# Performance work log

Measured on AMD Instinct MI355X. Metric: run time of the kernel, lower is better.

The kernel has to match this reference:

```python
import jax, jax.numpy as jnp
import numpy as np

B, S, H, K, L, NH, FF = 4, 2048, 2048, 1024, 2, 16, 4096
EPS = 1e-5

def _alibi_slopes(n):
    # standard power-of-two ALiBi slopes
    start = 2.0 ** (-8.0 / n)
    return start ** jnp.arange(1, n + 1, dtype=jnp.float32)

def _layernorm(h, g, b):
    mu = jnp.mean(h, axis=-1, keepdims=True)
    var = jnp.mean(jnp.square(h - mu), axis=-1, keepdims=True)
    return (h - mu) * jax.lax.rsqrt(var + EPS) * g + b

def setup_inputs() -> dict:
    key = jax.random.key(0)
    ks = jax.random.split(key, 16)
    x = jax.random.normal(ks[0], (B, S, H), jnp.float32)
    prev = jax.random.normal(ks[1], (B, S, H), jnp.float32)
    # unique sorted token indices per batch row (jit-friendly boolean mask)
    idx = jnp.stack([jnp.sort(jax.random.permutation(jax.random.fold_in(ks[2], b), S)[:K])
                     for b in range(B)]).astype(jnp.int32)
    w = 0.02
    Wq = jax.random.normal(ks[3], (L, H, H), jnp.float32) * w
    Wk = jax.random.normal(ks[4], (L, H, H), jnp.float32) * w
    Wv = jax.random.normal(ks[5], (L, H, H), jnp.float32) * w
    Wo = jax.random.normal(ks[6], (L, H, H), jnp.float32) * w
    attn_gamma = jnp.ones((L, H), jnp.float32)
    attn_beta = jnp.zeros((L, H), jnp.float32)
    mlp_gamma = jnp.ones((L, H), jnp.float32)
    mlp_beta = jnp.zeros((L, H), jnp.float32)
    Wgate = jax.random.normal(ks[7], (L, H, FF), jnp.float32) * w
    Wup = jax.random.normal(ks[8], (L, H, FF), jnp.float32) * w
    Wdown = jax.random.normal(ks[9], (L, FF, H), jnp.float32) * w
    return {"x": x, "prev": prev, "idx": idx, "Wq": Wq, "Wk": Wk, "Wv": Wv,
            "Wo": Wo, "attn_gamma": attn_gamma, "attn_beta": attn_beta,
            "mlp_gamma": mlp_gamma, "mlp_beta": mlp_beta,
            "Wgate": Wgate, "Wup": Wup, "Wdown": Wdown}

def _forward(x, prev, idx, Wq, Wk, Wv, Wo, attn_gamma, attn_beta,
             mlp_gamma, mlp_beta, Wgate, Wup, Wdown):
    d = H // NH
    scale = 1.0 / jnp.sqrt(jnp.asarray(d, jnp.float32))
    # gather selected tokens: [B, K, H]
    cur = jnp.take_along_axis(x, idx[:, :, None], axis=1)
    mem = jnp.take_along_axis(prev, idx[:, :, None], axis=1)
    # non-causal ALiBi bias over selected-sequence positions: [NH, K, K]
    pos = jnp.arange(K)
    dist = jnp.abs(pos[:, None] - pos[None, :]).astype(jnp.float32)
    bias = -_alibi_slopes(NH)[:, None, None] * dist
    for l in range(L):
        q = (cur @ Wq[l]).reshape(B, K, NH, d)
        k = (mem @ Wk[l]).reshape(B, K, NH, d)
        v = (mem @ Wv[l]).reshape(B, K, NH, d)
        scores = jnp.einsum('bqhd,bkhd->bhqk', q, k) * scale + bias
        attn = jax.nn.softmax(scores, axis=-1)
        o = jnp.einsum('bhqk,bkhd->bqhd', attn, v).reshape(B, K, H) @ Wo[l]
        cur = cur + o
        normed = _layernorm(cur, attn_gamma[l], attn_beta[l])
        mlp = (jax.nn.silu(normed @ Wgate[l]) * (normed @ Wup[l])) @ Wdown[l]
        cur = cur + mlp
        cur = _layernorm(cur, mlp_gamma[l], mlp_beta[l])
    # scatter-add back: out[mask] += update_val
    out = x.at[jnp.arange(B)[:, None], idx].add(cur)
    return out

def reference(x, prev, idx, Wq, Wk, Wv, Wo, attn_gamma, attn_beta,
              mlp_gamma, mlp_beta, Wgate, Wup, Wdown):
    return _forward(x, prev, idx, Wq, Wk, Wv, Wo, attn_gamma, attn_beta,
                    mlp_gamma, mlp_beta, Wgate, Wup, Wdown)
```

## Files before the change

kernel.cpp:

```cpp
#include <hip/hip_runtime.h>
#include <hip/hip_bf16.h>

#define BB 4
#define SS 2048
#define HH 2048
#define KK 1024
#define LL 2
#define NHH 16
#define FFF 4096
#define DD 128

typedef __attribute__((ext_vector_type(8))) short s8v;
typedef __attribute__((ext_vector_type(4))) short s4v;
typedef __attribute__((ext_vector_type(4))) float f4v;

__device__ __forceinline__ short f2bf(float f) {
  unsigned u = __builtin_bit_cast(unsigned, f);
  u += 0x7fffu + ((u >> 16) & 1u);
  return (short)(u >> 16);
}
__device__ __forceinline__ float bf2f(short s) {
  unsigned u = ((unsigned)(unsigned short)s) << 16;
  return __builtin_bit_cast(float, u);
}
__device__ __forceinline__ f4v mfma16(s8v a, s8v b, f4v c) {
  asm("v_mfma_f32_16x16x32_bf16 %0, %1, %2, %0" : "+v"(c) : "v"(a), "v"(b));
  return c;
}
__device__ __forceinline__ void gload_lds16(const void* g, void* l) {
  __builtin_amdgcn_global_load_lds(
      (__attribute__((address_space(1))) void*)g,
      (__attribute__((address_space(3))) void*)l, 16, 0, 0);
}
template <int N>
__device__ __forceinline__ void barrier_cnt() {
  if constexpr (N == 3)
    asm volatile("s_waitcnt vmcnt(3) expcnt(0) lgkmcnt(0)" ::: "memory");
  else if constexpr (N == 4)
    asm volatile("s_waitcnt vmcnt(4) expcnt(0) lgkmcnt(0)" ::: "memory");
  else
    asm volatile("s_waitcnt vmcnt(0) expcnt(0) lgkmcnt(0)" ::: "memory");
  __builtin_amdgcn_s_barrier();
  asm volatile("" ::: "memory");
}

__global__ __launch_bounds__(256) void wconv(const float* __restrict__ W,
                                             short* __restrict__ Wt,
                                             int Kd, int N) {
  __shared__ short tile[64][65];
  int n0 = blockIdx.x * 64, k0 = blockIdx.y * 64;
  int t = threadIdx.x;
#pragma unroll
  for (int i = 0; i < 16; ++i) {
    int lin = i * 256 + t;
    int r = lin >> 6, c = lin & 63;
    tile[c][r] = f2bf(W[(size_t)(k0 + r) * N + n0 + c]);
  }
  __syncthreads();
#pragma unroll
  for (int i = 0; i < 16; ++i) {
    int lin = i * 256 + t;
    int r = lin >> 6, c = lin & 63;
    Wt[(size_t)(n0 + r) * Kd + k0 + c] = tile[r][c];
  }
}

__global__ __launch_bounds__(256) void gather_rows(
    const float* __restrict__ x, const float* __restrict__ prev,
    const int* __restrict__ idx, float* __restrict__ cur_f,
    short* __restrict__ cur_b, short* __restrict__ mem_b) {
  int r = blockIdx.x;
  int b = r >> 10, kk = r & (KK - 1);
  int src = idx[b * KK + kk];
  const float4* xs = (const float4*)(x + ((size_t)b * SS + src) * HH);
  const float4* ps = (const float4*)(prev + ((size_t)b * SS + src) * HH);
  float4* cf = (float4*)(cur_f + (size_t)r * HH);
  s4v* cb = (s4v*)(cur_b + (size_t)r * HH);
  s4v* mb = (s4v*)(mem_b + (size_t)r * HH);
  int t = threadIdx.x;
#pragma unroll
  for (int i = 0; i < 2; ++i) {
    int c = t + i * 256;
    float4 xv = xs[c], pv = ps[c];
    cf[c] = xv;
    s4v cv, mv;
    cv[0] = f2bf(xv.x); cv[1] = f2bf(xv.y); cv[2] = f2bf(xv.z); cv[3] = f2bf(xv.w);
    mv[0] = f2bf(pv.x); mv[1] = f2bf(pv.y); mv[2] = f2bf(pv.z); mv[3] = f2bf(pv.w);
    cb[c] = cv; mb[c] = mv;
  }
}

template <int EPI>
__global__ __launch_bounds__(512, 2) void g8p(
    const short* __restrict__ A, const short* __restrict__ Bt,
    float* __restrict__ Cf, short* __restrict__ Cb,
    const short* __restrict__ Other, int M, int N, int Kd) {
  __shared__ __align__(16) short smem[3 * 12288];
  const int t = threadIdx.x;
  const int w = t >> 6, l = t & 63;
  const int wr = w >> 2, wc = w & 3;
  const int l15 = l & 15, lh = l >> 4;
  const int koffs = (lh ^ ((l15 >> 1) & 3)) * 8;

  const int gx = gridDim.x, gy = gridDim.y;
  const int nwg = gx * gy;
  const int bid = blockIdx.y * gx + blockIdx.x;
  const int wg = (bid & 7) * (nwg >> 3) + (bid >> 3);
  const int by = wg & (gy - 1);
  const int bx = wg / gy;
  const int rowBase = by * 128, colBase = bx * 256;

  const int ar = t >> 2;
  const int ac = ((t & 3) ^ ((t >> 3) & 3)) * 8;
  const short* gA = A + (size_t)(rowBase + ar) * Kd + ac;
  const short* gB0 = Bt + (size_t)(colBase + ar) * Kd + ac;
  const short* gB1 = gB0 + (size_t)128 * Kd;
  const int lA = t * 8;
  const int lB = 4096 + t * 8;

  auto stage = [&](int bi, int kt) {
    const int k0 = kt * 32;
    short* base = smem + bi * 12288;
    gload_lds16(gA + k0, base + lA);
    gload_lds16(gB0 + k0, base + lB);
    gload_lds16(gB1 + k0, base + lB + 4096);
  };

  f4v acc[4][4];
#pragma unroll
  for (int i = 0; i < 4; ++i)
#pragma unroll
    for (int j = 0; j < 4; ++j) acc[i][j] = (f4v){0.f, 0.f, 0.f, 0.f};

  const int NT = Kd >> 5;
  stage(0, 0);
  stage(1, 1);
  barrier_cnt<3>();

  int cur = 0;
  for (int kt = 0; kt < NT; ++kt) {
    const short* sb = smem + cur * 12288;
    const bool more = (kt + 2 < NT);
    if (more) {
      int nb = cur + 2; if (nb >= 3) nb -= 3;
      stage(nb, kt + 2);
    }
    s8v af[4], bf[4];
#pragma unroll
    for (int mt = 0; mt < 4; ++mt)
      af[mt] = *(const s8v*)(sb + (wr * 64 + mt * 16 + l15) * 32 + koffs);
#pragma unroll
    for (int nt = 0; nt < 4; ++nt)
      bf[nt] = *(const s8v*)(sb + 4096 + (wc * 64 + nt * 16 + l15) * 32 + koffs);
#pragma unroll
    for (int mt = 0; mt < 4; ++mt)
#pragma unroll
      for (int nt = 0; nt < 4; ++nt)
        acc[mt][nt] = mfma16(af[mt], bf[nt], acc[mt][nt]);
    if (more) barrier_cnt<3>(); else barrier_cnt<0>();
    cur = (cur + 1 == 3) ? 0 : cur + 1;
  }

#pragma unroll
  for (int mt = 0; mt < 4; ++mt) {
#pragma unroll
    for (int nt = 0; nt < 4; ++nt) {
#pragma unroll
      for (int rr = 0; rr < 4; ++rr) {
        int row = rowBase + wr * 64 + mt * 16 + lh * 4 + rr;
        int col = colBase + wc * 64 + nt * 16 + l15;
        float v = acc[mt][nt][rr];
        if constexpr (EPI == 0) {
          Cb[(size_t)row * N + col] = f2bf(v);
        } else if constexpr (EPI == 1) {
          Cf[(size_t)row * N + col] += v;
        } else if constexpr (EPI == 2) {
          int b = row >> 10, ktok = row & (KK - 1);
          int h = col >> 7, dd = col & (DD - 1);
          Cb[(((size_t)(b * NHH + h)) * DD + dd) * KK + ktok] = f2bf(v);
        } else if constexpr (EPI == 3) {
          float sv = v / (1.f + __expf(-v));
          Cb[(size_t)row * N + col] = f2bf(sv);
        } else {
          float o = bf2f(Other[(size_t)row * N + col]);
          Cb[(size_t)row * N + col] = f2bf(v * o);
        }
      }
    }
  }
}

template <int EPI>
__global__ __launch_bounds__(512, 2) void g256(
    const short* __restrict__ A, const short* __restrict__ Bt,
    float* __restrict__ Cf, short* __restrict__ Cb,
    const short* __restrict__ Other, int M, int N, int Kd) {
  __shared__ __align__(16) short smem[3 * 16384];
  const int t = threadIdx.x;
  const int w = t >> 6, l = t & 63;
  const int wr = w >> 1, wc = w & 1;
  const int l15 = l & 15, lh = l >> 4;
  const int koffs = (lh ^ ((l15 >> 1) & 3)) * 8;

  const int gx = gridDim.x, gy = gridDim.y;
  const int nwg = gx * gy;
  const int bid = blockIdx.y * gx + blockIdx.x;
  const int wg = (bid & 7) * (nwg >> 3) + (bid >> 3);
  const int by = wg & (gy - 1);
  const int bx = wg / gy;
  const int rowBase = by * 256, colBase = bx * 256;

  const int ar = t >> 2;
  const int ac = ((t & 3) ^ ((t >> 3) & 3)) * 8;
  const short* gA = A + (size_t)(rowBase + ar) * Kd + ac;
  const short* gB = Bt + (size_t)(colBase + ar) * Kd + ac;
  const int lA = t * 8;
  const int lB = 8192 + t * 8;

  auto stage = [&](int bi, int kt) {
    const int k0 = kt * 32;
    short* base = smem + bi * 16384;
    gload_lds16(gA + k0, base + lA);
    gload_lds16(gA + k0 + (size_t)128 * Kd, base + lA + 4096);
    gload_lds16(gB + k0, base + lB);
    gload_lds16(gB + k0 + (size_t)128 * Kd, base + lB + 4096);
  };

  f4v acc[4][8];
#pragma unroll
  for (int i = 0; i < 4; ++i)
#pragma unroll
    for (int j = 0; j < 8; ++j) acc[i][j] = (f4v){0.f, 0.f, 0.f, 0.f};

  const int NT = Kd >> 5;
  stage(0, 0);
  stage(1, 1);
  barrier_cnt<4>();

  int cur = 0;
  for (int kt = 0; kt < NT; ++kt) {
    const short* sb = smem + cur * 16384;
    const bool more = (kt + 2 < NT);
    if (more) {
      int nb = cur + 2; if (nb >= 3) nb -= 3;
      stage(nb, kt + 2);
    }
    s8v af[4], bf[8];
#pragma unroll
    for (int mt = 0; mt < 4; ++mt)
      af[mt] = *(const s8v*)(sb + (wr * 64 + mt * 16 + l15) * 32 + koffs);
#pragma unroll
    for (int nt = 0; nt < 8; ++nt)
      bf[nt] = *(const s8v*)(sb + 8192 + (wc * 128 + nt * 16 + l15) * 32 + koffs);
#pragma unroll
    for (int mt = 0; mt < 4; ++mt)
#pragma unroll
      for (int nt = 0; nt < 8; ++nt)
        acc[mt][nt] = mfma16(af[mt], bf[nt], acc[mt][nt]);
    if (more) barrier_cnt<4>(); else barrier_cnt<0>();
    cur = (cur + 1 == 3) ? 0 : cur + 1;
  }

#pragma unroll
  for (int mt = 0; mt < 4; ++mt) {
#pragma unroll
    for (int nt = 0; nt < 8; ++nt) {
#pragma unroll
      for (int rr = 0; rr < 4; ++rr) {
        int row = rowBase + wr * 64 + mt * 16 + lh * 4 + rr;
        int col = colBase + wc * 128 + nt * 16 + l15;
        float v = acc[mt][nt][rr];
        if constexpr (EPI == 0) {
          Cb[(size_t)row * N + col] = f2bf(v);
        } else if constexpr (EPI == 1) {
          Cf[(size_t)row * N + col] += v;
        } else if constexpr (EPI == 3) {
          float sv = v / (1.f + __expf(-v));
          Cb[(size_t)row * N + col] = f2bf(sv);
        } else if constexpr (EPI == 4) {
          float o = bf2f(Other[(size_t)row * N + col]);
          Cb[(size_t)row * N + col] = f2bf(v * o);
        }
      }
    }
  }
}

__global__ __launch_bounds__(256, 2) void attn_fwd(
    const short* __restrict__ qb, const short* __restrict__ kb,
    const short* __restrict__ vT, short* __restrict__ ob) {
  __shared__ __align__(16) short Kl[64 * 136];
  __shared__ __align__(16) short Vl[128 * 72];
  __shared__ __align__(16) short Pl[64 * 72];
  int b = blockIdx.z, h = blockIdx.y, qt = blockIdx.x;
  int t = threadIdx.x, w = t >> 6, l = t & 63, l15 = l & 15, lh = l >> 4;
  const float LOG2E = 1.4426950408889634f;
  float slope2 = exp2f(-0.5f * (float)(h + 1)) * LOG2E;
  const float c1 = 0.08838834764831845f * LOG2E;

  s8v qf[4];
  int qrowA = qt * 64 + w * 16 + l15;
  const short* qptr = qb + ((size_t)(b * KK + qrowA)) * HH + h * DD + lh * 8;
#pragma unroll
  for (int ks = 0; ks < 4; ++ks) qf[ks] = *(const s8v*)(qptr + ks * 32);

  f4v oacc[8];
#pragma unroll
  for (int i = 0; i < 8; ++i) oacc[i] = (f4v){0.f, 0.f, 0.f, 0.f};
  float m[4], sden[4];
#pragma unroll
  for (int r = 0; r < 4; ++r) { m[r] = -1e30f; sden[r] = 0.f; }
  int qpos_base = qt * 64 + w * 16 + lh * 4;

  for (int kt = 0; kt < KK / 64; ++kt) {
    {
      int rr = t >> 4, cc = (t & 15) * 8;
#pragma unroll
      for (int it = 0; it < 4; ++it) {
        int krow = it * 16 + rr;
        s8v g = *(const s8v*)(kb + ((size_t)(b * KK + kt * 64 + krow)) * HH + h * DD + cc);
        *(s8v*)&Kl[krow * 136 + cc] = g;
      }
      int dr = t >> 3, c2 = (t & 7) * 8;
#pragma unroll
      for (int it = 0; it < 4; ++it) {
        int drow = it * 32 + dr;
        s8v g = *(const s8v*)(vT + (((size_t)(b * NHH + h)) * DD + drow) * KK + kt * 64 + c2);
        *(s8v*)&Vl[drow * 72 + c2] = g;
      }
    }
    __syncthreads();

    f4v sacc[4];
#pragma unroll
    for (int ct = 0; ct < 4; ++ct) sacc[ct] = (f4v){0.f, 0.f, 0.f, 0.f};
#pragma unroll
    for (int ct = 0; ct < 4; ++ct)
#pragma unroll
      for (int ks = 0; ks < 4; ++ks) {
        s8v kf = *(const s8v*)&Kl[(ct * 16 + l15) * 136 + ks * 32 + lh * 8];
        sacc[ct] = mfma16(qf[ks], kf, sacc[ct]);
      }

#pragma unroll
    for (int r = 0; r < 4; ++r) {
      int qpos = qpos_base + r;
      float mx = -1e30f;
#pragma unroll
      for (int ct = 0; ct < 4; ++ct) {
        int kpos = kt * 64 + ct * 16 + l15;
        float sv = sacc[ct][r] * c1 - slope2 * fabsf((float)(qpos - kpos));
        sacc[ct][r] = sv;
        mx = fmaxf(mx, sv);
      }
      mx = fmaxf(mx, __shfl_xor(mx, 1));
      mx = fmaxf(mx, __shfl_xor(mx, 2));
      mx = fmaxf(mx, __shfl_xor(mx, 4));
      mx = fmaxf(mx, __shfl_xor(mx, 8));
      float mn = fmaxf(m[r], mx);
      float corr = exp2f(m[r] - mn);
      m[r] = mn;
      float ps = 0.f;
#pragma unroll
      for (int ct = 0; ct < 4; ++ct) {
        float p = exp2f(sacc[ct][r] - mn);
        sacc[ct][r] = p;
        ps += p;
      }
      ps += __shfl_xor(ps, 1); ps += __shfl_xor(ps, 2);
      ps += __shfl_xor(ps, 4); ps += __shfl_xor(ps, 8);
      sden[r] = sden[r] * corr + ps;
#pragma unroll
      for (int dt = 0; dt < 8; ++dt) oacc[dt][r] *= corr;
#pragma unroll
      for (int ct = 0; ct < 4; ++ct)
        Pl[(w * 16 + lh * 4 + r) * 72 + ct * 16 + l15] = f2bf(sacc[ct][r]);
    }

#pragma unroll
    for (int ks2 = 0; ks2 < 2; ++ks2) {
      s8v pa = *(const s8v*)&Pl[(w * 16 + l15) * 72 + ks2 * 32 + lh * 8];
#pragma unroll
      for (int dt = 0; dt < 8; ++dt) {
        s8v vf = *(const s8v*)&Vl[(dt * 16 + l15) * 72 + ks2 * 32 + lh * 8];
        oacc[dt] = mfma16(pa, vf, oacc[dt]);
      }
    }
    __syncthreads();
  }

#pragma unroll
  for (int dt = 0; dt < 8; ++dt)
#pragma unroll
    for (int r = 0; r < 4; ++r) {
      int qpos = qpos_base + r;
      int dd = dt * 16 + l15;
      ob[((size_t)(b * KK + qpos)) * HH + h * DD + dd] = f2bf(oacc[dt][r] / sden[r]);
    }
}

__global__ __launch_bounds__(256) void ln_rows(const float* in,
    const float* __restrict__ gma, const float* __restrict__ bta,
    short* __restrict__ outb, float* outf) {
  __shared__ float red[2][4];
  int r = blockIdx.x, t = threadIdx.x;
  const float4* x4 = (const float4*)(in + (size_t)r * HH);
  float4 va = x4[t], vb = x4[t + 256];
  float sum = va.x + va.y + va.z + va.w + vb.x + vb.y + vb.z + vb.w;
  float sq = va.x * va.x + va.y * va.y + va.z * va.z + va.w * va.w +
             vb.x * vb.x + vb.y * vb.y + vb.z * vb.z + vb.w * vb.w;
#pragma unroll
  for (int off = 32; off; off >>= 1) {
    sum += __shfl_down(sum, off);
    sq += __shfl_down(sq, off);
  }
  int w = t >> 6;
  if ((t & 63) == 0) { red[0][w] = sum; red[1][w] = sq; }
  __syncthreads();
  sum = red[0][0] + red[0][1] + red[0][2] + red[0][3];
  sq = red[1][0] + red[1][1] + red[1][2] + red[1][3];
  float mu = sum * (1.f / HH);
  float rs = rsqrtf(sq * (1.f / HH) - mu * mu + 1e-5f);
  const float4* g4 = (const float4*)gma;
  const float4* b4 = (const float4*)bta;
  s4v* ob = (s4v*)(outb + (size_t)r * HH);
  float4* of = (float4*)(outf ? outf + (size_t)r * HH : nullptr);
#pragma unroll
  for (int i = 0; i < 2; ++i) {
    int c = t + i * 256;
    float4 v = (i == 0) ? va : vb;
    float4 g = g4[c], bb = b4[c];
    float4 nv;
    nv.x = (v.x - mu) * rs * g.x + bb.x;
    nv.y = (v.y - mu) * rs * g.y + bb.y;
    nv.z = (v.z - mu) * rs * g.z + bb.z;
    nv.w = (v.w - mu) * rs * g.w + bb.w;
    s4v o;
    o[0] = f2bf(nv.x); o[1] = f2bf(nv.y); o[2] = f2bf(nv.z); o[3] = f2bf(nv.w);
    ob[c] = o;
    if (outf) of[c] = nv;
  }
}

__global__ __launch_bounds__(256) void copy_out(const float* __restrict__ x,
                                                float* __restrict__ out, size_t n4) {
  size_t i = (size_t)blockIdx.x * 256 + threadIdx.x;
  size_t stride = (size_t)gridDim.x * 256;
  const float4* xi = (const float4*)x;
  float4* oi = (float4*)out;
  for (; i < n4; i += stride) oi[i] = xi[i];
}

__global__ __launch_bounds__(256) void scatter_add(const int* __restrict__ idx,
                                                   const float* __restrict__ cur,
                                                   float* out) {
  int r = blockIdx.x;
  int b = r >> 10, kk = r & (KK - 1);
  int dst = idx[b * KK + kk];
  float4* o = (float4*)(out + ((size_t)b * SS + dst) * HH);
  const float4* c = (const float4*)(cur + (size_t)r * HH);
  int t = threadIdx.x;
#pragma unroll
  for (int i = 0; i < 2; ++i) {
    int j = t + i * 256;
    float4 ov = o[j], cv = c[j];
    ov.x += cv.x; ov.y += cv.y; ov.z += cv.z; ov.w += cv.w;
    o[j] = ov;
  }
}

extern "C" void kernel_launch(void* const* d_in, const int* in_sizes, int n_in,
                              void* d_out, int out_size, void* d_ws, size_t ws_size,
                              hipStream_t stream) {
  (void)in_sizes; (void)n_in; (void)out_size; (void)ws_size;
  const float* x = (const float*)d_in[0];
  const float* prv = (const float*)d_in[1];
  const int* idx = (const int*)d_in[2];
  const float* Wq = (const float*)d_in[3];
  const float* Wk = (const float*)d_in[4];
  const float* Wv = (const float*)d_in[5];
  const float* Wo = (const float*)d_in[6];
  const float* ag = (const float*)d_in[7];
  const float* ab = (const float*)d_in[8];
  const float* mg = (const float*)d_in[9];
  const float* mbt = (const float*)d_in[10];
  const float* Wg = (const float*)d_in[11];
  const float* Wu = (const float*)d_in[12];
  const float* Wd = (const float*)d_in[13];
  float* out = (float*)d_out;

  char* ws = (char*)d_ws;
  size_t off = 0;
  auto alloc = [&](size_t bytes) -> void* {
    void* p = ws + off;
    off += (bytes + 255) & ~(size_t)255;
    return p;
  };
  const size_t WHH = (size_t)HH * HH, WHF = (size_t)HH * FFF;
  short* WqT = (short*)alloc(LL * WHH * 2);
  short* WkT = (short*)alloc(LL * WHH * 2);
  short* WvT = (short*)alloc(LL * WHH * 2);
  short* WoT = (short*)alloc(LL * WHH * 2);
  short* WgT = (short*)alloc(LL * WHF * 2);
  short* WuT = (short*)alloc(LL * WHF * 2);
  short* WdT = (short*)alloc(LL * WHF * 2);
  const size_t RH = (size_t)BB * KK * HH;
  float* cur_f = (float*)alloc(RH * 4);
  short* q_b = (short*)alloc(RH * 2);
  short* k_b = (short*)alloc(RH * 2);
  short* vT_b = (short*)alloc(RH * 2);
  short* o_b = (short*)alloc(RH * 2);
  short* cur_b = (short*)alloc(RH * 2);
  short* mem_b = (short*)alloc(RH * 2);
  short* nrm_b = (short*)alloc(RH * 2);
  short* sg_b = q_b;
  short* hid_b = vT_b;

  dim3 blk(256), blk512(512);
  for (int l = 0; l < LL; ++l) {
    wconv<<<dim3(HH / 64, HH / 64), blk, 0, stream>>>(Wq + l * WHH, WqT + l * WHH, HH, HH);
    wconv<<<dim3(HH / 64, HH / 64), blk, 0, stream>>>(Wk + l * WHH, WkT + l * WHH, HH, HH);
    wconv<<<dim3(HH / 64, HH / 64), blk, 0, stream>>>(Wv + l * WHH, WvT + l * WHH, HH, HH);
    wconv<<<dim3(HH / 64, HH / 64), blk, 0, stream>>>(Wo + l * WHH, WoT + l * WHH, HH, HH);
    wconv<<<dim3(FFF / 64, HH / 64), blk, 0, stream>>>(Wg + l * WHF, WgT + l * WHF, HH, FFF);
    wconv<<<dim3(FFF / 64, HH / 64), blk, 0, stream>>>(Wu + l * WHF, WuT + l * WHF, HH, FFF);
    wconv<<<dim3(HH / 64, FFF / 64), blk, 0, stream>>>(Wd + l * WHF, WdT + l * WHF, FFF, HH);
  }
  gather_rows<<<dim3(BB * KK), blk, 0, stream>>>(x, prv, idx, cur_f, cur_b, mem_b);

  const int M = BB * KK;
  for (int l = 0; l < LL; ++l) {
    const short* wq = WqT + l * WHH;
    const short* wk = WkT + l * WHH;
    const short* wv = WvT + l * WHH;
    const short* wo = WoT + l * WHH;
    const short* wg_ = WgT + l * WHF;
    const short* wu = WuT + l * WHF;
    const short* wd = WdT + l * WHF;
    g8p<0><<<dim3(HH / 256, M / 128), blk512, 0, stream>>>(cur_b, wq, nullptr, q_b, nullptr, M, HH, HH);
    g8p<0><<<dim3(HH / 256, M / 128), blk512, 0, stream>>>(mem_b, wk, nullptr, k_b, nullptr, M, HH, HH);
    g8p<2><<<dim3(HH / 256, M / 128), blk512, 0, stream>>>(mem_b, wv, nullptr, vT_b, nullptr, M, HH, HH);
    attn_fwd<<<dim3(KK / 64, NHH, BB), blk, 0, stream>>>(q_b, k_b, vT_b, o_b);
    g8p<1><<<dim3(HH / 256, M / 128), blk512, 0, stream>>>(o_b, wo, cur_f, nullptr, nullptr, M, HH, HH);
    ln_rows<<<dim3(M), blk, 0, stream>>>(cur_f, ag + l * HH, ab + l * HH, nrm_b, nullptr);
    g256<3><<<dim3(FFF / 256, M / 256), blk512, 0, stream>>>(nrm_b, wg_, nullptr, sg_b, nullptr, M, FFF, HH);
    g256<4><<<dim3(FFF / 256, M / 256), blk512, 0, stream>>>(nrm_b, wu, nullptr, hid_b, sg_b, M, FFF, HH);
    g8p<1><<<dim3(HH / 256, M / 128), blk512, 0, stream>>>(hid_b, wd, cur_f, nullptr, nullptr, M, HH, FFF);
    ln_rows<<<dim3(M), blk, 0, stream>>>(cur_f, mg + l * HH, mbt + l * HH, cur_b, cur_f);
  }
  copy_out<<<dim3(2048), blk, 0, stream>>>(x, out, (size_t)BB * SS * HH / 4);
  scatter_add<<<dim3(M), blk, 0, stream>>>(idx, cur_f, out);
}
```

Measured before the change: 1.309 ms.

## Fuse K/V and gate/up projections into single wide GEMMs, use fast exp2

Result: no change. 1.319 ms (+0.8%).

```diff
diff --git a/kernel.cpp b/kernel.cpp
--- a/kernel.cpp
+++ b/kernel.cpp
@@ -94,7 +94,7 @@
 __global__ __launch_bounds__(512, 2) void g8p(
     const short* __restrict__ A, const short* __restrict__ Bt,
     float* __restrict__ Cf, short* __restrict__ Cb,
-    const short* __restrict__ Other, int M, int N, int Kd) {
+    int M, int N, int Kd) {
   __shared__ __align__(16) short smem[3 * 12288];
   const int t = threadIdx.x;
   const int w = t >> 6, l = t & 63;
@@ -178,12 +178,6 @@
           int b = row >> 10, ktok = row & (KK - 1);
           int h = col >> 7, dd = col & (DD - 1);
           Cb[(((size_t)(b * NHH + h)) * DD + dd) * KK + ktok] = f2bf(v);
-        } else if constexpr (EPI == 3) {
-          float sv = v / (1.f + __expf(-v));
-          Cb[(size_t)row * N + col] = f2bf(sv);
-        } else {
-          float o = bf2f(Other[(size_t)row * N + col]);
-          Cb[(size_t)row * N + col] = f2bf(v * o);
         }
       }
     }
@@ -193,8 +187,7 @@
 template <int EPI>
 __global__ __launch_bounds__(512, 2) void g256(
     const short* __restrict__ A, const short* __restrict__ Bt,
-    float* __restrict__ Cf, short* __restrict__ Cb,
-    const short* __restrict__ Other, int M, int N, int Kd) {
+    short* __restrict__ Cb, short* __restrict__ Cb2, int M, int N, int Kd) {
   __shared__ __align__(16) short smem[3 * 16384];
   const int t = threadIdx.x;
   const int w = t >> 6, l = t & 63;
@@ -270,22 +263,48 @@
         int row = rowBase + wr * 64 + mt * 16 + lh * 4 + rr;
         int col = colBase + wc * 128 + nt * 16 + l15;
         float v = acc[mt][nt][rr];
-        if constexpr (EPI == 0) {
-          Cb[(size_t)row * N + col] = f2bf(v);
-        } else if constexpr (EPI == 1) {
-          Cf[(size_t)row * N + col] += v;
-        } else if constexpr (EPI == 3) {
-          float sv = v / (1.f + __expf(-v));
-          Cb[(size_t)row * N + col] = f2bf(sv);
-        } else if constexpr (EPI == 4) {
-          float o = bf2f(Other[(size_t)row * N + col]);
-          Cb[(size_t)row * N + col] = f2bf(v * o);
+        if constexpr (EPI == 5) {
+          if (col < HH) {
+            Cb[(size_t)row * HH + col] = f2bf(v);
+          } else {
+            int vcol = col - HH;
+            int b = row >> 10, ktok = row & (KK - 1);
+            int h = vcol >> 7, dd = vcol & (DD - 1);
+            Cb2[(((size_t)(b * NHH + h)) * DD + dd) * KK + ktok] = f2bf(v);
+          }
+        } else if constexpr (EPI == 6) {
+          if (col < FFF) {
+            float sv = v / (1.f + __expf(-v));
+            Cb[(size_t)row * FFF + col] = f2bf(sv);
+          } else {
+            Cb2[(size_t)row * FFF + (col - FFF)] = f2bf(v);
+          }
         }
       }
     }
   }
 }
 
+__global__ __launch_bounds__(256) void mul_bf16(short* __restrict__ hid,
+                                                const short* __restrict__ sg,
+                                                size_t n8) {
+  size_t i = (size_t)blockIdx.x * 256 + threadIdx.x;
+  size_t stride = (size_t)gridDim.x * 256;
+  for (; i < n8; i += stride) {
+    s8v a = ((const s8v*)hid)[i];
+    s8v b = ((const s8v*)sg)[i];
+    s8v o;
+#pragma unroll
+    for (int j = 0; j < 8; ++j) o[j] = f2bf(bf2f(a[j]) * bf2f(b[j]));
+    ((s8v*)hid)[i] = o;
+  }
+}
+
+__device__ __forceinline__ float exp2fast(float x) {
+  float r;
+  asm("v_exp_f32 %0, %1\n\ts_nop 0" : "=v"(r) : "v"(x));
+  return r;
+}
 __global__ __launch_bounds__(256, 2) void attn_fwd(
     const short* __restrict__ qb, const short* __restrict__ kb,
     const short* __restrict__ vT, short* __restrict__ ob) {
@@ -358,12 +377,12 @@
       mx = fmaxf(mx, __shfl_xor(mx, 4));
       mx = fmaxf(mx, __shfl_xor(mx, 8));
       float mn = fmaxf(m[r], mx);
-      float corr = exp2f(m[r] - mn);
+      float corr = exp2fast(m[r] - mn);
       m[r] = mn;
       float ps = 0.f;
 #pragma unroll
       for (int ct = 0; ct < 4; ++ct) {
-        float p = exp2f(sacc[ct][r] - mn);
+        float p = exp2fast(sacc[ct][r] - mn);
         sacc[ct][r] = p;
         ps += p;
       }
@@ -498,11 +517,9 @@
   };
   const size_t WHH = (size_t)HH * HH, WHF = (size_t)HH * FFF;
   short* WqT = (short*)alloc(LL * WHH * 2);
-  short* WkT = (short*)alloc(LL * WHH * 2);
-  short* WvT = (short*)alloc(LL * WHH * 2);
+  short* WkvT = (short*)alloc(LL * 2 * WHH * 2);
   short* WoT = (short*)alloc(LL * WHH * 2);
-  short* WgT = (short*)alloc(LL * WHF * 2);
-  short* WuT = (short*)alloc(LL * WHF * 2);
+  short* WguT = (short*)alloc(LL * 2 * WHF * 2);
   short* WdT = (short*)alloc(LL * WHF * 2);
   const size_t RH = (size_t)BB * KK * HH;
   float* cur_f = (float*)alloc(RH * 4);
@@ -519,11 +536,11 @@
   dim3 blk(256), blk512(512);
   for (int l = 0; l < LL; ++l) {
     wconv<<<dim3(HH / 64, HH / 64), blk, 0, stream>>>(Wq + l * WHH, WqT + l * WHH, HH, HH);
-    wconv<<<dim3(HH / 64, HH / 64), blk, 0, stream>>>(Wk + l * WHH, WkT + l * WHH, HH, HH);
-    wconv<<<dim3(HH / 64, HH / 64), blk, 0, stream>>>(Wv + l * WHH, WvT + l * WHH, HH, HH);
+    wconv<<<dim3(HH / 64, HH / 64), blk, 0, stream>>>(Wk + l * WHH, WkvT + l * 2 * WHH, HH, HH);
+    wconv<<<dim3(HH / 64, HH / 64), blk, 0, stream>>>(Wv + l * WHH, WkvT + l * 2 * WHH + WHH, HH, HH);
     wconv<<<dim3(HH / 64, HH / 64), blk, 0, stream>>>(Wo + l * WHH, WoT + l * WHH, HH, HH);
-    wconv<<<dim3(FFF / 64, HH / 64), blk, 0, stream>>>(Wg + l * WHF, WgT + l * WHF, HH, FFF);
-    wconv<<<dim3(FFF / 64, HH / 64), blk, 0, stream>>>(Wu + l * WHF, WuT + l * WHF, HH, FFF);
+    wconv<<<dim3(FFF / 64, HH / 64), blk, 0, stream>>>(Wg + l * WHF, WguT + l * 2 * WHF, HH, FFF);
+    wconv<<<dim3(FFF / 64, HH / 64), blk, 0, stream>>>(Wu + l * WHF, WguT + l * 2 * WHF + WHF, HH, FFF);
     wconv<<<dim3(HH / 64, FFF / 64), blk, 0, stream>>>(Wd + l * WHF, WdT + l * WHF, FFF, HH);
   }
   gather_rows<<<dim3(BB * KK), blk, 0, stream>>>(x, prv, idx, cur_f, cur_b, mem_b);
@@ -531,21 +548,18 @@
   const int M = BB * KK;
   for (int l = 0; l < LL; ++l) {
     const short* wq = WqT + l * WHH;
-    const short* wk = WkT + l * WHH;
-    const short* wv = WvT + l * WHH;
+    const short* wkv = WkvT + l * 2 * WHH;
     const short* wo = WoT + l * WHH;
-    const short* wg_ = WgT + l * WHF;
-    const short* wu = WuT + l * WHF;
+    const short* wgu = WguT + l * 2 * WHF;
     const short* wd = WdT + l * WHF;
-    g8p<0><<<dim3(HH / 256, M / 128), blk512, 0, stream>>>(cur_b, wq, nullptr, q_b, nullptr, M, HH, HH);
-    g8p<0><<<dim3(HH / 256, M / 128), blk512, 0, stream>>>(mem_b, wk, nullptr, k_b, nullptr, M, HH, HH);
-    g8p<2><<<dim3(HH / 256, M / 128), blk512, 0, stream>>>(mem_b, wv, nullptr, vT_b, nullptr, M, HH, HH);
+    g8p<0><<<dim3(HH / 256, M / 128), blk512, 0, stream>>>(cur_b, wq, nullptr, q_b, M, HH, HH);
+    g256<5><<<dim3(2 * HH / 256, M / 256), blk512, 0, stream>>>(mem_b, wkv, k_b, vT_b, M, 2 * HH, HH);
     attn_fwd<<<dim3(KK / 64, NHH, BB), blk, 0, stream>>>(q_b, k_b, vT_b, o_b);
-    g8p<1><<<dim3(HH / 256, M / 128), blk512, 0, stream>>>(o_b, wo, cur_f, nullptr, nullptr, M, HH, HH);
+    g8p<1><<<dim3(HH / 256, M / 128), blk512, 0, stream>>>(o_b, wo, cur_f, nullptr, M, HH, HH);
     ln_rows<<<dim3(M), blk, 0, stream>>>(cur_f, ag + l * HH, ab + l * HH, nrm_b, nullptr);
-    g256<3><<<dim3(FFF / 256, M / 256), blk512, 0, stream>>>(nrm_b, wg_, nullptr, sg_b, nullptr, M, FFF, HH);
-    g256<4><<<dim3(FFF / 256, M / 256), blk512, 0, stream>>>(nrm_b, wu, nullptr, hid_b, sg_b, M, FFF, HH);
-    g8p<1><<<dim3(HH / 256, M / 128), blk512, 0, stream>>>(hid_b, wd, cur_f, nullptr, nullptr, M, HH, FFF);
+    g256<6><<<dim3(2 * FFF / 256, M / 256), blk512, 0, stream>>>(nrm_b, wgu, sg_b, hid_b, M, 2 * FFF, HH);
+    mul_bf16<<<dim3(2048), blk, 0, stream>>>(hid_b, sg_b, RH * 2 / 8);
+    g8p<1><<<dim3(HH / 256, M / 128), blk512, 0, stream>>>(hid_b, wd, cur_f, nullptr, M, HH, FFF);
     ln_rows<<<dim3(M), blk, 0, stream>>>(cur_f, mg + l * HH, mbt + l * HH, cur_b, cur_f);
   }
   copy_out<<<dim3(2048), blk, 0, stream>>>(x, out, (size_t)BB * SS * HH / 4);
```
